# Kernel tuning notes

Measured on AMD Instinct MI355X. Metric: run time of the kernel, lower is better.

## Reference

```python
import jax, jax.numpy as jnp
import numpy as np

N_P, E_P = 50000, 400000
N_L, E_L = 50000, 400000
B = 256  # number of graphs per side
NEG_GAT = 0.2   # GATv2 leaky-relu slope
NEG_FC = 0.01   # nn.LeakyReLU default slope


def _gatv2(x, ei, Wl, Wr, att, b, H, C):
    """GATv2Conv (concat heads, add_self_loops=True). Wl/Wr: [in, H*C], att: [H, C], b: [H*C]."""
    N = x.shape[0]
    sl = jnp.arange(N)
    src = jnp.concatenate([ei[0], sl])
    dst = jnp.concatenate([ei[1], sl])
    xl = (x @ Wl).reshape(N, H, C)   # source transform (messages)
    xr = (x @ Wr).reshape(N, H, C)   # target transform
    e = jax.nn.leaky_relu(xl[src] + xr[dst], NEG_GAT)          # [E+N, H, C]
    logits = jnp.einsum('ehc,hc->eh', e, att)                   # [E+N, H]
    m = jax.ops.segment_max(logits, dst, num_segments=N)        # segment softmax
    a = jnp.exp(logits - m[dst])
    alpha = a / jax.ops.segment_sum(a, dst, num_segments=N)[dst]
    out = jax.ops.segment_sum(xl[src] * alpha[..., None], dst, num_segments=N)
    return out.reshape(N, H * C) + b


def _mean_pool(x, batch, nb):
    s = jax.ops.segment_sum(x, batch, num_segments=nb)
    c = jax.ops.segment_sum(jnp.ones((x.shape[0],), x.dtype), batch, num_segments=nb)
    return s / jnp.maximum(c, 1.0)[:, None]


def setup_inputs() -> dict:
    key = jax.random.key(0)
    ks = jax.random.split(key, 48)
    i = [0]
    def nrm(shape, fan_in):
        k = ks[i[0]]; i[0] += 1
        return jax.random.normal(k, shape, jnp.float32) / np.sqrt(fan_in)
    inp = {}
    inp['protein_x'] = jax.random.normal(ks[40], (N_P, 10), jnp.float32)
    inp['ligand_x'] = jax.random.normal(ks[41], (N_L, 5), jnp.float32)
    inp['protein_edge_index'] = jax.random.randint(ks[42], (2, E_P), 0, N_P)
    inp['ligand_edge_index'] = jax.random.randint(ks[43], (2, E_L), 0, N_L)
    inp['protein_batch'] = (jnp.arange(N_P) * B) // N_P  # sorted graph ids, all segments nonempty
    inp['ligand_batch'] = (jnp.arange(N_L) * B) // N_L
    # GATv2 params: layer1 heads=2 out=128, layer2 heads=1 out=256
    inp['p1_Wl'] = nrm((10, 256), 10); inp['p1_Wr'] = nrm((10, 256), 10)
    inp['p1_att'] = nrm((2, 128), 128); inp['p1_b'] = jnp.zeros((256,), jnp.float32)
    inp['p2_Wl'] = nrm((256, 256), 256); inp['p2_Wr'] = nrm((256, 256), 256)
    inp['p2_att'] = nrm((1, 256), 256); inp['p2_b'] = jnp.zeros((256,), jnp.float32)
    inp['l1_Wl'] = nrm((5, 256), 5); inp['l1_Wr'] = nrm((5, 256), 5)
    inp['l1_att'] = nrm((2, 128), 128); inp['l1_b'] = jnp.zeros((256,), jnp.float32)
    inp['l2_Wl'] = nrm((256, 256), 256); inp['l2_Wr'] = nrm((256, 256), 256)
    inp['l2_att'] = nrm((1, 256), 256); inp['l2_b'] = jnp.zeros((256,), jnp.float32)
    # MultiheadAttention(256, 4) params ([in, out] convention)
    inp['Wq'] = nrm((256, 256), 256); inp['bq'] = jnp.zeros((256,), jnp.float32)
    inp['Wk'] = nrm((256, 256), 256); inp['bk'] = jnp.zeros((256,), jnp.float32)
    inp['Wv'] = nrm((256, 256), 256); inp['bv'] = jnp.zeros((256,), jnp.float32)
    inp['Wo'] = nrm((256, 256), 256); inp['bo'] = jnp.zeros((256,), jnp.float32)
    # fc head
    inp['fc1_w'] = nrm((512, 256), 512); inp['fc1_b'] = jnp.zeros((256,), jnp.float32)
    inp['ln_g'] = jnp.ones((256,), jnp.float32); inp['ln_b'] = jnp.zeros((256,), jnp.float32)
    inp['fc2_w'] = nrm((256, 1), 256); inp['fc2_b'] = jnp.zeros((1,), jnp.float32)
    return inp


def reference(protein_x, protein_edge_index, protein_batch,
              ligand_x, ligand_edge_index, ligand_batch,
              p1_Wl, p1_Wr, p1_att, p1_b, p2_Wl, p2_Wr, p2_att, p2_b,
              l1_Wl, l1_Wr, l1_att, l1_b, l2_Wl, l2_Wr, l2_att, l2_b,
              Wq, bq, Wk, bk, Wv, bv, Wo, bo,
              fc1_w, fc1_b, ln_g, ln_b, fc2_w, fc2_b):
    px = _gatv2(protein_x, protein_edge_index, p1_Wl, p1_Wr, p1_att, p1_b, 2, 128)
    px = _gatv2(px, protein_edge_index, p2_Wl, p2_Wr, p2_att, p2_b, 1, 256)
    px = _mean_pool(px, protein_batch, B)                        # [B, 256]
    lx = _gatv2(ligand_x, ligand_edge_index, l1_Wl, l1_Wr, l1_att, l1_b, 2, 128)
    lx = _gatv2(lx, ligand_edge_index, l2_Wl, l2_Wr, l2_att, l2_b, 1, 256)
    lx = _mean_pool(lx, ligand_batch, B)                         # [B, 256]
    # cross attention with q/k/v seq length 1
    D, H = 256, 4
    d = D // H
    qh = (px @ Wq + bq).reshape(B, H, d)
    kh = (lx @ Wk + bk).reshape(B, H, d)
    vh = (lx @ Wv + bv).reshape(B, H, d)
    scores = (qh * kh).sum(-1) / jnp.sqrt(jnp.float32(d))        # [B, H], 1 key
    w = jax.nn.softmax(scores[..., None], axis=-1)               # all ones (single key)
    attn = (w * vh).reshape(B, D) @ Wo + bo                      # [B, 256]
    comb = jnp.concatenate([px, attn], axis=1)                   # [B, 512]
    h = comb @ fc1_w + fc1_b
    mu = h.mean(-1, keepdims=True)
    var = h.var(-1, keepdims=True)
    h = (h - mu) / jnp.sqrt(var + 1e-5) * ln_g + ln_b
    h = jax.nn.leaky_relu(h, NEG_FC)
    return h @ fc2_w + fc2_b                                     # [B, 1]
```

## Files before the change

kernel.cpp:

```cpp
#include <hip/hip_runtime.h>
#include <math.h>

typedef unsigned short u16;
typedef __attribute__((ext_vector_type(8))) short bf16x8;
typedef __attribute__((ext_vector_type(4))) float f32x4;

__device__ inline u16 f2bf(float x) {
  unsigned int u = __float_as_uint(x);
  u += 0x7fffu + ((u >> 16) & 1u);
  return (u16)(u >> 16);
}
__device__ inline float bf2f(u16 h) {
  return __uint_as_float(((unsigned int)h) << 16);
}
__device__ inline float4 ld_bf4(const u16* p) {
  ushort4 v = *(const ushort4*)p;
  return make_float4(bf2f(v.x), bf2f(v.y), bf2f(v.z), bf2f(v.w));
}

__global__ void k_setup(int* __restrict__ cnt, int nz,
                        const float* __restrict__ Wpl, const float* __restrict__ Wpr,
                        const float* __restrict__ Wll, const float* __restrict__ Wlr,
                        u16* __restrict__ Whp, u16* __restrict__ Wlp,
                        u16* __restrict__ Whl, u16* __restrict__ Wll_o) {
  const int zb = (nz + 255) / 256;
  if ((int)blockIdx.x < zb) {
    int i = blockIdx.x * 256 + threadIdx.x;
    if (i < nz) cnt[i] = 0;
    return;
  }
  int wb = blockIdx.x - zb;
  int n = wb & 511;
  int side = wb >> 9;
  int col = n & 255;
  int k = threadIdx.x;
  const float* W = side == 0 ? (n < 256 ? Wpl : Wpr) : (n < 256 ? Wll : Wlr);
  float w = W[k * 256 + col];
  u16* Wh = side ? Whl : Whp;
  u16* Wlo = side ? Wll_o : Wlp;
  u16 hb = f2bf(w);
  Wh[n * 256 + k] = hb;
  Wlo[n * 256 + k] = f2bf(w - bf2f(hb));
}

__global__ void k_histb(const int* __restrict__ eip, int Ep, const int* __restrict__ eil,
                        int El, int* __restrict__ cntp, int* __restrict__ cntl) {
  int e = blockIdx.x * blockDim.x + threadIdx.x;
  if (e < Ep) atomicAdd(&cntp[eip[Ep + e]], 1);
  else if (e < Ep + El) { int e2 = e - Ep; atomicAdd(&cntl[eil[El + e2]], 1); }
}

__global__ void k_scan1b(const int* __restrict__ cntp, int Np, const int* __restrict__ cntl,
                         int Nl, int nbp, int* __restrict__ offsp, int* __restrict__ offsl,
                         int* __restrict__ curp, int* __restrict__ curl,
                         int* __restrict__ bsum) {
  __shared__ int s[256];
  int tid = threadIdx.x;
  int side = ((int)blockIdx.x >= nbp) ? 1 : 0;
  int blk = side ? (blockIdx.x - nbp) : blockIdx.x;
  const int* cnt = side ? cntl : cntp;
  int* offs = side ? offsl : offsp;
  int* cur = side ? curl : curp;
  int N = side ? Nl : Np;
  int i = blk * 256 + tid;
  int v = (i < N) ? cnt[i] : 0;
  if (i < N) cur[i] = 0;
  s[tid] = v;
  __syncthreads();
  for (int off = 1; off < 256; off <<= 1) {
    int t = 0;
    if (tid >= off) t = s[tid - off];
    __syncthreads();
    if (tid >= off) s[tid] += t;
    __syncthreads();
  }
  if (i < N) offs[i] = s[tid] - v;
  if (tid == 255) bsum[side * 256 + blk] = s[255];
}

__global__ void k_scan2b(int* __restrict__ bsum, int nbp, int nbl) {
  __shared__ int s[256];
  int side = blockIdx.x;
  int nb = side ? nbl : nbp;
  int* bs = bsum + side * 256;
  int tid = threadIdx.x;
  int v = (tid < nb) ? bs[tid] : 0;
  s[tid] = v;
  __syncthreads();
  for (int off = 1; off < 256; off <<= 1) {
    int t = 0;
    if (tid >= off) t = s[tid - off];
    __syncthreads();
    if (tid >= off) s[tid] += t;
    __syncthreads();
  }
  if (tid < nb) bs[tid] = s[tid] - v;
}

__global__ void k_fillb(const int* __restrict__ eip, int Ep, const int* __restrict__ eil,
                        int El, const int* __restrict__ offsp, const int* __restrict__ offsl,
                        const int* __restrict__ bsum,
                        int* __restrict__ curp, int* __restrict__ curl,
                        int* __restrict__ csrp, int* __restrict__ csrl) {
  int e = blockIdx.x * blockDim.x + threadIdx.x;
  if (e < Ep) {
    int d = eip[Ep + e];
    int pos = offsp[d] + bsum[d >> 8] + atomicAdd(&curp[d], 1);
    csrp[pos] = eip[e];
  } else if (e < Ep + El) {
    int e2 = e - Ep;
    int d = eil[El + e2];
    int pos = offsl[d] + bsum[256 + (d >> 8)] + atomicAdd(&curl[d], 1);
    csrl[pos] = eil[e2];
  }
}

__global__ void k_lin_small_b(const float* __restrict__ xp, int Kp, int Np,
                              const float* __restrict__ xl_, int Kl, int Nl,
                              const float* __restrict__ Wpl, const float* __restrict__ Wpr,
                              const float* __restrict__ Wll, const float* __restrict__ Wlr,
                              u16* __restrict__ xlh_p, u16* __restrict__ xrh_p,
                              u16* __restrict__ xlh_l, u16* __restrict__ xrh_l) {
  const int side = blockIdx.y;
  const float* x = side ? xl_ : xp;
  const int K = side ? Kl : Kp;
  const int N = side ? Nl : Np;
  const float* Wl = side ? Wll : Wpl;
  const float* Wr = side ? Wlr : Wpr;
  u16* xlh = side ? xlh_l : xlh_p;
  u16* xrh = side ? xrh_l : xrh_p;
  int base = blockIdx.x * 8;
  if (base >= N) return;
  int j = threadIdx.x;
  __shared__ float xs[8][16];
  int tot = 8 * K;
  for (int i = j; i < tot; i += 256) {
    int r = i / K, k = i - r * K;
    if (base + r < N) xs[r][k] = x[(size_t)(base + r) * K + k];
  }
  __syncthreads();
#pragma unroll
  for (int r = 0; r < 8; ++r) {
    int n = base + r;
    if (n >= N) break;
    float al = 0.f, ar = 0.f;
    for (int k = 0; k < K; ++k) {
      float xv = xs[r][k];
      al = fmaf(xv, Wl[k * 256 + j], al);
      ar = fmaf(xv, Wr[k * 256 + j], ar);
    }
    xlh[(size_t)n * 256 + j] = f2bf(al);
    xrh[(size_t)n * 256 + j] = f2bf(ar);
  }
}

__global__ void __launch_bounds__(256, 2) k_mm_dual_b(
    const u16* __restrict__ A_p, const u16* __restrict__ A_l,
    const u16* __restrict__ Bh_p, const u16* __restrict__ Bl_p,
    const u16* __restrict__ Bh_l, const u16* __restrict__ Bl_l,
    u16* __restrict__ XLh_p, u16* __restrict__ XRh_p,
    u16* __restrict__ XLh_l, u16* __restrict__ XRh_l, int Np, int Nl) {
  __shared__ __align__(16) char smem[32768];
  char* sA = smem;
  char* sBh = smem + 8192;
  char* sBl = smem + 16384;
  const int side = blockIdx.z;
  const u16* A = side ? A_l : A_p;
  const u16* Bhi = side ? Bh_l : Bh_p;
  const u16* Blo = side ? Bl_l : Bl_p;
  u16* XLh = side ? XLh_l : XLh_p;
  u16* XRh = side ? XRh_l : XRh_p;
  const int M = side ? Nl : Np;
  const int t = threadIdx.x;
  const int rowBase = blockIdx.x * 128;
  if (rowBase >= M) return;
  const int j0 = blockIdx.y * 128;
  const int srow = t >> 1;
  const int h = t & 1;
  int gr = rowBase + srow;
  if (gr >= M) gr = M - 1;
  const size_t gaBase = (size_t)gr * 256 + h * 16;
  const size_t gbBase = (size_t)(j0 + srow) * 256 + h * 16;
  const int rb = srow * 64;
  const int sw0 = (((h * 2) + (srow >> 1)) & 3) * 16;
  const int sw1 = (((h * 2 + 1) + (srow >> 1)) & 3) * 16;
  const int lane = t & 63;
  const int wid = t >> 6;
  const int wm = (wid & 1) * 64;
  const int wn = (wid >> 1) * 64;
  const int kq = lane >> 4;
  const int mr = lane & 15;
  int offA[4], offB[4];
#pragma unroll
  for (int i = 0; i < 4; ++i) {
    int m = wm + i * 16 + mr;
    offA[i] = m * 64 + ((kq + (m >> 1)) & 3) * 16;
    int n = wn + i * 16 + mr;
    offB[i] = n * 64 + ((kq + (n >> 1)) & 3) * 16;
  }
  f32x4 acc[4][4] = {};
  for (int kt = 0; kt < 8; ++kt) {
    const int k0 = kt * 32;
    uint4 va0 = *(const uint4*)(A + gaBase + k0);
    uint4 va1 = *(const uint4*)(A + gaBase + k0 + 8);
    uint4 vbh0 = *(const uint4*)(Bhi + gbBase + k0);
    uint4 vbh1 = *(const uint4*)(Bhi + gbBase + k0 + 8);
    uint4 vbl0 = *(const uint4*)(Blo + gbBase + k0);
    uint4 vbl1 = *(const uint4*)(Blo + gbBase + k0 + 8);
    __syncthreads();
    *(uint4*)(sA + rb + sw0) = va0;
    *(uint4*)(sA + rb + sw1) = va1;
    *(uint4*)(sBh + rb + sw0) = vbh0;
    *(uint4*)(sBh + rb + sw1) = vbh1;
    *(uint4*)(sBl + rb + sw0) = vbl0;
    *(uint4*)(sBl + rb + sw1) = vbl1;
    __syncthreads();
    bf16x8 a[4], bh[4], bl[4];
#pragma unroll
    for (int i = 0; i < 4; ++i) {
      a[i] = *(const bf16x8*)(sA + offA[i]);
      bh[i] = *(const bf16x8*)(sBh + offB[i]);
      bl[i] = *(const bf16x8*)(sBl + offB[i]);
    }
#pragma unroll
    for (int i = 0; i < 4; ++i)
#pragma unroll
      for (int j = 0; j < 4; ++j) {
        acc[i][j] = __builtin_amdgcn_mfma_f32_16x16x32_bf16(a[i], bh[j], acc[i][j], 0, 0, 0);
        acc[i][j] = __builtin_amdgcn_mfma_f32_16x16x32_bf16(a[i], bl[j], acc[i][j], 0, 0, 0);
      }
  }
  __syncthreads();
  u16* wtile = (u16*)(smem + wid * 8192);
#pragma unroll
  for (int i = 0; i < 4; ++i)
#pragma unroll
    for (int j = 0; j < 4; ++j)
#pragma unroll
      for (int r = 0; r < 4; ++r)
        wtile[(i * 16 + kq * 4 + r) * 64 + j * 16 + mr] = f2bf(acc[i][j][r]);
  u16* cbase = (blockIdx.y < 2) ? XLh : XRh;
  const int cb = (blockIdx.y < 2) ? j0 : j0 - 256;
  const int r8 = lane >> 3;
  const int c8 = lane & 7;
#pragma unroll
  for (int rr = 0; rr < 8; ++rr) {
    int lr = rr * 8 + r8;
    uint4 v = *(const uint4*)&wtile[lr * 64 + c8 * 8];
    int row = rowBase + wm + lr;
    if (row < M) *(uint4*)&cbase[(size_t)row * 256 + cb + wn + c8 * 8] = v;
  }
}

#define GAT_DOT(a, q)                                                        \
  {                                                                          \
    float t0 = a.x + rd.x, t1 = a.y + rd.y, t2 = a.z + rd.z, t3 = a.w + rd.w; \
    q = fmaf(fmaxf(t0, 0.2f * t0), wa.x,                                     \
        fmaf(fmaxf(t1, 0.2f * t1), wa.y,                                     \
        fmaf(fmaxf(t2, 0.2f * t2), wa.z, fmaxf(t3, 0.2f * t3) * wa.w)));     \
  }

template <int H>
__global__ void k_gat_gather_b(
    const u16* __restrict__ xlh_p, const u16* __restrict__ xrh_p, u16* __restrict__ out_p,
    const u16* __restrict__ xlh_l, const u16* __restrict__ xrh_l, u16* __restrict__ out_l,
    const int* __restrict__ csr_p, const int* __restrict__ offs_p,
    const int* __restrict__ cnt_p,
    const int* __restrict__ csr_l, const int* __restrict__ offs_l,
    const int* __restrict__ cnt_l, const int* __restrict__ bsum,
    const float* __restrict__ att_p, const float* __restrict__ bias_p,
    const float* __restrict__ att_l, const float* __restrict__ bias_l,
    int Np, int Nl) {
  const int side = blockIdx.y;
  const u16* xlh = side ? xlh_l : xlh_p;
  const u16* xrh = side ? xrh_l : xrh_p;
  u16* out = side ? out_l : out_p;
  const int* csr = side ? csr_l : csr_p;
  const int* offs = side ? offs_l : offs_p;
  const int* cnt = side ? cnt_l : cnt_p;
  const float* att = side ? att_l : att_p;
  const float* bias = side ? bias_l : bias_p;
  const int N = side ? Nl : Np;
  int d = blockIdx.x * 4 + (threadIdx.x >> 6);
  if (d >= N) return;
  const int lo4 = (threadIdx.x & 63) * 4;
  const float4 rd = ld_bf4(&xrh[(size_t)d * 256 + lo4]);
  const float4 wa = *(const float4*)&att[lo4];
  const float4 xd = ld_bf4(&xlh[(size_t)d * 256 + lo4]);
  float base;
  GAT_DOT(xd, base)
#pragma unroll
  for (int off = 1; off <= (H == 2 ? 16 : 32); off <<= 1) base += __shfl_xor(base, off, 64);
  float l0 = 1.f, l1 = 0.f, l2 = 0.f, l3 = 0.f;
  float4 acc0 = xd;
  float4 acc1 = make_float4(0.f, 0.f, 0.f, 0.f);
  float4 acc2 = make_float4(0.f, 0.f, 0.f, 0.f);
  float4 acc3 = make_float4(0.f, 0.f, 0.f, 0.f);
  const int o0 = offs[d] + bsum[side * 256 + (d >> 8)];
  const int c = cnt[d];
  int j = 0;
  for (; j + 3 < c; j += 4) {
    int s0 = csr[o0 + j], s1 = csr[o0 + j + 1], s2 = csr[o0 + j + 2], s3 = csr[o0 + j + 3];
    float4 a0 = ld_bf4(&xlh[(size_t)s0 * 256 + lo4]);
    float4 a1 = ld_bf4(&xlh[(size_t)s1 * 256 + lo4]);
    float4 a2 = ld_bf4(&xlh[(size_t)s2 * 256 + lo4]);
    float4 a3 = ld_bf4(&xlh[(size_t)s3 * 256 + lo4]);
    float q0, q1, q2, q3;
    GAT_DOT(a0, q0)
    GAT_DOT(a1, q1)
    GAT_DOT(a2, q2)
    GAT_DOT(a3, q3)
#pragma unroll
    for (int off = 1; off <= (H == 2 ? 16 : 32); off <<= 1) {
      q0 += __shfl_xor(q0, off, 64);
      q1 += __shfl_xor(q1, off, 64);
      q2 += __shfl_xor(q2, off, 64);
      q3 += __shfl_xor(q3, off, 64);
    }
    float w0 = __expf(q0 - base), w1 = __expf(q1 - base);
    float w2 = __expf(q2 - base), w3 = __expf(q3 - base);
    l0 += w0; l1 += w1; l2 += w2; l3 += w3;
    acc0.x = fmaf(w0, a0.x, acc0.x); acc0.y = fmaf(w0, a0.y, acc0.y);
    acc0.z = fmaf(w0, a0.z, acc0.z); acc0.w = fmaf(w0, a0.w, acc0.w);
    acc1.x = fmaf(w1, a1.x, acc1.x); acc1.y = fmaf(w1, a1.y, acc1.y);
    acc1.z = fmaf(w1, a1.z, acc1.z); acc1.w = fmaf(w1, a1.w, acc1.w);
    acc2.x = fmaf(w2, a2.x, acc2.x); acc2.y = fmaf(w2, a2.y, acc2.y);
    acc2.z = fmaf(w2, a2.z, acc2.z); acc2.w = fmaf(w2, a2.w, acc2.w);
    acc3.x = fmaf(w3, a3.x, acc3.x); acc3.y = fmaf(w3, a3.y, acc3.y);
    acc3.z = fmaf(w3, a3.z, acc3.z); acc3.w = fmaf(w3, a3.w, acc3.w);
  }
  for (; j < c; ++j) {
    int s0 = csr[o0 + j];
    float4 a0 = ld_bf4(&xlh[(size_t)s0 * 256 + lo4]);
    float q0;
    GAT_DOT(a0, q0)
#pragma unroll
    for (int off = 1; off <= (H == 2 ? 16 : 32); off <<= 1) q0 += __shfl_xor(q0, off, 64);
    float w0 = __expf(q0 - base);
    l0 += w0;
    acc0.x = fmaf(w0, a0.x, acc0.x); acc0.y = fmaf(w0, a0.y, acc0.y);
    acc0.z = fmaf(w0, a0.z, acc0.z); acc0.w = fmaf(w0, a0.w, acc0.w);
  }
  float inv = 1.f / (l0 + l1 + l2 + l3);
  float ax = acc0.x + acc1.x + acc2.x + acc3.x;
  float ay = acc0.y + acc1.y + acc2.y + acc3.y;
  float az = acc0.z + acc1.z + acc2.z + acc3.z;
  float aw = acc0.w + acc1.w + acc2.w + acc3.w;
  const float4 b4 = *(const float4*)&bias[lo4];
  ushort4 hv;
  hv.x = f2bf(ax * inv + b4.x);
  hv.y = f2bf(ay * inv + b4.y);
  hv.z = f2bf(az * inv + b4.z);
  hv.w = f2bf(aw * inv + b4.w);
  *(ushort4*)&out[(size_t)d * 256 + lo4] = hv;
}

#define POOL_C 8
__global__ void k_pool_part(const u16* __restrict__ xp, const int* __restrict__ bp, int Np,
                            const u16* __restrict__ xl_, const int* __restrict__ bl_, int Nl,
                            float* __restrict__ PPpart, float* __restrict__ LPpart) {
  const int b = blockIdx.x;
  const int side = blockIdx.y;
  const int chunk = blockIdx.z;
  const u16* x = side ? xl_ : xp;
  const int* batch = side ? bl_ : bp;
  const int N = side ? Nl : Np;
  float* part = side ? LPpart : PPpart;
  int j = threadIdx.x;
  __shared__ int sss, sse;
  if (j == 0) {
    int lo = 0, hi = N;
    while (lo < hi) { int mid = (lo + hi) >> 1; if (batch[mid] < b) lo = mid + 1; else hi = mid; }
    sss = lo;
    lo = 0; hi = N;
    while (lo < hi) { int mid = (lo + hi) >> 1; if (batch[mid] < b + 1) lo = mid + 1; else hi = mid; }
    sse = lo;
  }
  __syncthreads();
  int len = sse - sss;
  int per = (len + POOL_C - 1) / POOL_C;
  int st = sss + chunk * per;
  int en = st + per;
  if (en > sse) en = sse;
  float acc = 0.f;
  for (int n = st; n < en; ++n) acc += bf2f(x[(size_t)n * 256 + j]);
  part[((size_t)chunk * 256 + b) * 256 + j] = acc;
}

__global__ void k_head(const float* __restrict__ PPpart, const float* __restrict__ LPpart,
                       const int* __restrict__ bp, int Np,
                       const int* __restrict__ bl_, int Nl,
                       const float* __restrict__ Wv, const float* __restrict__ bv,
                       const float* __restrict__ Wo, const float* __restrict__ bo,
                       const float* __restrict__ fc1w, const float* __restrict__ fc1b,
                       const float* __restrict__ lng, const float* __restrict__ lnb,
                       const float* __restrict__ fc2w, const float* __restrict__ fc2b,
                       float* __restrict__ out) {
  int b = blockIdx.x;
  int j = threadIdx.x;
  __shared__ float lxs[256];
  __shared__ float vbuf[256];
  __shared__ float comb[512];
  __shared__ float r1[256], r2[256];
  __shared__ float smu, srs;
  __shared__ int seg[4];
  if (j < 2) {
    const int* batch = j ? bl_ : bp;
    int N = j ? Nl : Np;
    int lo = 0, hi = N;
    while (lo < hi) { int mid = (lo + hi) >> 1; if (batch[mid] < b) lo = mid + 1; else hi = mid; }
    seg[j * 2] = lo;
    lo = 0; hi = N;
    while (lo < hi) { int mid = (lo + hi) >> 1; if (batch[mid] < b + 1) lo = mid + 1; else hi = mid; }
    seg[j * 2 + 1] = lo;
  }
  __syncthreads();
  {
    float accp = 0.f, accl = 0.f;
#pragma unroll
    for (int c = 0; c < POOL_C; ++c) {
      accp += PPpart[((size_t)c * 256 + b) * 256 + j];
      accl += LPpart[((size_t)c * 256 + b) * 256 + j];
    }
    comb[j] = accp / fmaxf((float)(seg[1] - seg[0]), 1.f);
    lxs[j] = accl / fmaxf((float)(seg[3] - seg[2]), 1.f);
  }
  __syncthreads();
  float v = bv[j];
  for (int k = 0; k < 256; ++k) v = fmaf(lxs[k], Wv[k * 256 + j], v);
  vbuf[j] = v;
  __syncthreads();
  float at = bo[j];
  for (int k = 0; k < 256; ++k) at = fmaf(vbuf[k], Wo[k * 256 + j], at);
  comb[256 + j] = at;
  __syncthreads();
  float h = fc1b[j];
  for (int k = 0; k < 512; ++k) h = fmaf(comb[k], fc1w[k * 256 + j], h);
  r1[j] = h;
  r2[j] = h * h;
  __syncthreads();
  for (int off = 128; off > 0; off >>= 1) {
    if (j < off) { r1[j] += r1[j + off]; r2[j] += r2[j + off]; }
    __syncthreads();
  }
  if (j == 0) {
    float mu = r1[0] / 256.f;
    float var = r2[0] / 256.f - mu * mu;
    smu = mu;
    srs = 1.f / sqrtf(var + 1e-5f);
  }
  __syncthreads();
  float hn = (h - smu) * srs * lng[j] + lnb[j];
  hn = hn > 0.f ? hn : 0.01f * hn;
  r1[j] = hn * fc2w[j];
  __syncthreads();
  for (int off = 128; off > 0; off >>= 1) {
    if (j < off) r1[j] += r1[j + off];
    __syncthreads();
  }
  if (j == 0) out[b] = r1[0] + fc2b[0];
}

extern "C" void kernel_launch(void* const* d_in, const int* in_sizes, int n_in,
                              void* d_out, int out_size, void* d_ws, size_t ws_size,
                              hipStream_t stream) {
  const float* px = (const float*)d_in[0];
  const float* lx = (const float*)d_in[1];
  const int* pei = (const int*)d_in[2];
  const int* lei = (const int*)d_in[3];
  const int* pb = (const int*)d_in[4];
  const int* lb = (const int*)d_in[5];
  const float* p1_Wl = (const float*)d_in[6];
  const float* p1_Wr = (const float*)d_in[7];
  const float* p1_att = (const float*)d_in[8];
  const float* p1_b = (const float*)d_in[9];
  const float* p2_Wl = (const float*)d_in[10];
  const float* p2_Wr = (const float*)d_in[11];
  const float* p2_att = (const float*)d_in[12];
  const float* p2_b = (const float*)d_in[13];
  const float* l1_Wl = (const float*)d_in[14];
  const float* l1_Wr = (const float*)d_in[15];
  const float* l1_att = (const float*)d_in[16];
  const float* l1_b = (const float*)d_in[17];
  const float* l2_Wl = (const float*)d_in[18];
  const float* l2_Wr = (const float*)d_in[19];
  const float* l2_att = (const float*)d_in[20];
  const float* l2_b = (const float*)d_in[21];
  const float* Wv = (const float*)d_in[26];
  const float* bv = (const float*)d_in[27];
  const float* Wo = (const float*)d_in[28];
  const float* bo = (const float*)d_in[29];
  const float* fc1w = (const float*)d_in[30];
  const float* fc1b = (const float*)d_in[31];
  const float* lng = (const float*)d_in[32];
  const float* lnb = (const float*)d_in[33];
  const float* fc2w = (const float*)d_in[34];
  const float* fc2b = (const float*)d_in[35];

  const int NPn = in_sizes[4];
  const int NLn = in_sizes[5];
  const int EPe = in_sizes[2] / 2;
  const int ELe = in_sizes[3] / 2;
  const int KP = in_sizes[0] / NPn;
  const int KL = in_sizes[1] / NLn;

  const int Nmax = NPn > NLn ? NPn : NLn;
  const int Emax = EPe > ELe ? EPe : ELe;
  size_t NF = (size_t)Nmax * 256;

  u16* XLh_p = (u16*)d_ws;
  u16* XRh_p = XLh_p + NF;
  u16* Ah_p = XRh_p + NF;
  u16* XLh_l = Ah_p + NF;
  u16* XRh_l = XLh_l + NF;
  u16* Ah_l = XRh_l + NF;
  u16* Wth = Ah_l + NF;
  u16* Wtl = Wth + 2 * 512 * 256;
  float* PPpart = (float*)(Wtl + 2 * 512 * 256);
  float* LPpart = PPpart + (size_t)POOL_C * 256 * 256;
  int* cnt = (int*)(LPpart + (size_t)POOL_C * 256 * 256);
  int* cur = cnt + 2 * (size_t)Nmax;
  int* offs = cur + 2 * (size_t)Nmax;
  int* bsum = offs + 2 * (size_t)Nmax;
  int* csr = bsum + 512;
  int* cnt_l = cnt + Nmax;
  int* cur_l = cur + Nmax;
  int* offs_l = offs + Nmax;
  int* csr_l = csr + Emax;

  const int nbp = (NPn + 255) / 256;
  const int nbl = (NLn + 255) / 256;
  const int nz = 2 * Nmax;
  const int zb = (nz + 255) / 256;

  k_setup<<<zb + 1024, 256, 0, stream>>>(cnt, nz, p2_Wl, p2_Wr, l2_Wl, l2_Wr,
                                         Wth, Wtl, Wth + 512 * 256, Wtl + 512 * 256);
  k_histb<<<(EPe + ELe + 255) / 256, 256, 0, stream>>>(pei, EPe, lei, ELe, cnt, cnt_l);
  k_scan1b<<<nbp + nbl, 256, 0, stream>>>(cnt, NPn, cnt_l, NLn, nbp, offs, offs_l,
                                          cur, cur_l, bsum);
  k_scan2b<<<2, 256, 0, stream>>>(bsum, nbp, nbl);
  k_fillb<<<(EPe + ELe + 255) / 256, 256, 0, stream>>>(pei, EPe, lei, ELe, offs, offs_l,
                                                       bsum, cur, cur_l, csr, csr_l);
  k_lin_small_b<<<dim3((Nmax + 7) / 8, 2), 256, 0, stream>>>(
      px, KP, NPn, lx, KL, NLn, p1_Wl, p1_Wr, l1_Wl, l1_Wr,
      XLh_p, XRh_p, XLh_l, XRh_l);
  k_gat_gather_b<2><<<dim3((Nmax + 3) / 4, 2), 256, 0, stream>>>(
      XLh_p, XRh_p, Ah_p, XLh_l, XRh_l, Ah_l,
      csr, offs, cnt, csr_l, offs_l, cnt_l, bsum,
      p1_att, p1_b, l1_att, l1_b, NPn, NLn);
  k_mm_dual_b<<<dim3((Nmax + 127) / 128, 4, 2), 256, 0, stream>>>(
      Ah_p, Ah_l, Wth, Wtl, Wth + 512 * 256, Wtl + 512 * 256,
      XLh_p, XRh_p, XLh_l, XRh_l, NPn, NLn);
  k_gat_gather_b<1><<<dim3((Nmax + 3) / 4, 2), 256, 0, stream>>>(
      XLh_p, XRh_p, Ah_p, XLh_l, XRh_l, Ah_l,
      csr, offs, cnt, csr_l, offs_l, cnt_l, bsum,
      p2_att, p2_b, l2_att, l2_b, NPn, NLn);
  k_pool_part<<<dim3(256, 2, POOL_C), 256, 0, stream>>>(Ah_p, pb, NPn, Ah_l, lb, NLn,
                                                        PPpart, LPpart);
  k_head<<<256, 256, 0, stream>>>(PPpart, LPpart, pb, NPn, lb, NLn,
                                  Wv, bv, Wo, bo, fc1w, fc1b, lng, lnb, fc2w, fc2b,
                                  (float*)d_out);
  (void)n_in; (void)out_size; (void)ws_size;
}
```

Before: 596.8 us.

## Widen GEMM N-tile to 256 and rewrite GATv2 leaky-relu dot via abs identity

The dual-bf16 GEMM block now computes a 128x256 output tile instead of 128x128, halving the grid's N dimension. This lets each A tile be reused across twice as many columns, and each warp now holds a 4x8 accumulator array with a two-chunk epilogue. The cost is more registers and more shared memory per block, which may cut occupancy. Separately, the leaky-relu-times-attention dot is rewritten as 0.6*t + 0.4*|t|, with scaled attention weights precomputed, so it uses fewer ALU ops in the gather loop.

```diff
diff --git a/kernel.cpp b/kernel.cpp
--- a/kernel.cpp
+++ b/kernel.cpp
@@ -160,104 +160,116 @@
     const u16* __restrict__ Bh_l, const u16* __restrict__ Bl_l,
     u16* __restrict__ XLh_p, u16* __restrict__ XRh_p,
     u16* __restrict__ XLh_l, u16* __restrict__ XRh_l, int Np, int Nl) {
-  __shared__ __align__(16) char smem[32768];
+  __shared__ __align__(16) char smem[40960];
   char* sA = smem;
   char* sBh = smem + 8192;
-  char* sBl = smem + 16384;
+  char* sBl = smem + 24576;
   const int side = blockIdx.z;
   const u16* A = side ? A_l : A_p;
   const u16* Bhi = side ? Bh_l : Bh_p;
   const u16* Blo = side ? Bl_l : Bl_p;
-  u16* XLh = side ? XLh_l : XLh_p;
-  u16* XRh = side ? XRh_l : XRh_p;
   const int M = side ? Nl : Np;
   const int t = threadIdx.x;
   const int rowBase = blockIdx.x * 128;
   if (rowBase >= M) return;
-  const int j0 = blockIdx.y * 128;
+  const int nsel = blockIdx.y;
   const int srow = t >> 1;
   const int h = t & 1;
   int gr = rowBase + srow;
   if (gr >= M) gr = M - 1;
   const size_t gaBase = (size_t)gr * 256 + h * 16;
-  const size_t gbBase = (size_t)(j0 + srow) * 256 + h * 16;
-  const int rb = srow * 64;
-  const int sw0 = (((h * 2) + (srow >> 1)) & 3) * 16;
-  const int sw1 = (((h * 2 + 1) + (srow >> 1)) & 3) * 16;
+  const int rbA = srow * 64;
+  const int swA0 = (((h * 2) + (srow >> 1)) & 3) * 16;
+  const int swA1 = (((h * 2 + 1) + (srow >> 1)) & 3) * 16;
+  const size_t gbBase = (size_t)(nsel * 256 + t) * 256;
+  const int rbB = t * 64;
+  int swB[4];
+#pragma unroll
+  for (int q = 0; q < 4; ++q) swB[q] = ((q + (t >> 1)) & 3) * 16;
   const int lane = t & 63;
   const int wid = t >> 6;
   const int wm = (wid & 1) * 64;
-  const int wn = (wid >> 1) * 64;
+  const int wn = (wid >> 1) * 128;
   const int kq = lane >> 4;
   const int mr = lane & 15;
-  int offA[4], offB[4];
+  int offA[4], offB[8];
 #pragma unroll
   for (int i = 0; i < 4; ++i) {
     int m = wm + i * 16 + mr;
     offA[i] = m * 64 + ((kq + (m >> 1)) & 3) * 16;
-    int n = wn + i * 16 + mr;
-    offB[i] = n * 64 + ((kq + (n >> 1)) & 3) * 16;
-  }
-  f32x4 acc[4][4] = {};
+  }
+#pragma unroll
+  for (int j = 0; j < 8; ++j) {
+    int n = wn + j * 16 + mr;
+    offB[j] = n * 64 + ((kq + (n >> 1)) & 3) * 16;
+  }
+  f32x4 acc[4][8] = {};
   for (int kt = 0; kt < 8; ++kt) {
     const int k0 = kt * 32;
     uint4 va0 = *(const uint4*)(A + gaBase + k0);
     uint4 va1 = *(const uint4*)(A + gaBase + k0 + 8);
-    uint4 vbh0 = *(const uint4*)(Bhi + gbBase + k0);
-    uint4 vbh1 = *(const uint4*)(Bhi + gbBase + k0 + 8);
-    uint4 vbl0 = *(const uint4*)(Blo + gbBase + k0);
-    uint4 vbl1 = *(const uint4*)(Blo + gbBase + k0 + 8);
-    __syncthreads();
-    *(uint4*)(sA + rb + sw0) = va0;
-    *(uint4*)(sA + rb + sw1) = va1;
-    *(uint4*)(sBh + rb + sw0) = vbh0;
-    *(uint4*)(sBh + rb + sw1) = vbh1;
-    *(uint4*)(sBl + rb + sw0) = vbl0;
-    *(uint4*)(sBl + rb + sw1) = vbl1;
-    __syncthreads();
-    bf16x8 a[4], bh[4], bl[4];
-#pragma unroll
-    for (int i = 0; i < 4; ++i) {
-      a[i] = *(const bf16x8*)(sA + offA[i]);
-      bh[i] = *(const bf16x8*)(sBh + offB[i]);
-      bl[i] = *(const bf16x8*)(sBl + offB[i]);
-    }
-#pragma unroll
-    for (int i = 0; i < 4; ++i)
-#pragma unroll
-      for (int j = 0; j < 4; ++j) {
-        acc[i][j] = __builtin_amdgcn_mfma_f32_16x16x32_bf16(a[i], bh[j], acc[i][j], 0, 0, 0);
-        acc[i][j] = __builtin_amdgcn_mfma_f32_16x16x32_bf16(a[i], bl[j], acc[i][j], 0, 0, 0);
+    uint4 vbh[4], vbl[4];
+#pragma unroll
+    for (int q = 0; q < 4; ++q) {
+      vbh[q] = *(const uint4*)(Bhi + gbBase + k0 + q * 8);
+      vbl[q] = *(const uint4*)(Blo + gbBase + k0 + q * 8);
+    }
+    __syncthreads();
+    *(uint4*)(sA + rbA + swA0) = va0;
+    *(uint4*)(sA + rbA + swA1) = va1;
+#pragma unroll
+    for (int q = 0; q < 4; ++q) {
+      *(uint4*)(sBh + rbB + swB[q]) = vbh[q];
+      *(uint4*)(sBl + rbB + swB[q]) = vbl[q];
+    }
+    __syncthreads();
+    bf16x8 a[4];
+#pragma unroll
+    for (int i = 0; i < 4; ++i) a[i] = *(const bf16x8*)(sA + offA[i]);
+#pragma unroll
+    for (int j = 0; j < 8; ++j) {
+      bf16x8 bh = *(const bf16x8*)(sBh + offB[j]);
+      bf16x8 bl = *(const bf16x8*)(sBl + offB[j]);
+#pragma unroll
+      for (int i = 0; i < 4; ++i) {
+        acc[i][j] = __builtin_amdgcn_mfma_f32_16x16x32_bf16(a[i], bh, acc[i][j], 0, 0, 0);
+        acc[i][j] = __builtin_amdgcn_mfma_f32_16x16x32_bf16(a[i], bl, acc[i][j], 0, 0, 0);
       }
+    }
   }
   __syncthreads();
   u16* wtile = (u16*)(smem + wid * 8192);
-#pragma unroll
-  for (int i = 0; i < 4; ++i)
-#pragma unroll
-    for (int j = 0; j < 4; ++j)
-#pragma unroll
-      for (int r = 0; r < 4; ++r)
-        wtile[(i * 16 + kq * 4 + r) * 64 + j * 16 + mr] = f2bf(acc[i][j][r]);
-  u16* cbase = (blockIdx.y < 2) ? XLh : XRh;
-  const int cb = (blockIdx.y < 2) ? j0 : j0 - 256;
+  u16* cbase = nsel ? (side ? XRh_l : XRh_p) : (side ? XLh_l : XLh_p);
   const int r8 = lane >> 3;
   const int c8 = lane & 7;
 #pragma unroll
-  for (int rr = 0; rr < 8; ++rr) {
-    int lr = rr * 8 + r8;
-    uint4 v = *(const uint4*)&wtile[lr * 64 + c8 * 8];
-    int row = rowBase + wm + lr;
-    if (row < M) *(uint4*)&cbase[(size_t)row * 256 + cb + wn + c8 * 8] = v;
-  }
-}
-
-#define GAT_DOT(a, q)                                                        \
-  {                                                                          \
-    float t0 = a.x + rd.x, t1 = a.y + rd.y, t2 = a.z + rd.z, t3 = a.w + rd.w; \
-    q = fmaf(fmaxf(t0, 0.2f * t0), wa.x,                                     \
-        fmaf(fmaxf(t1, 0.2f * t1), wa.y,                                     \
-        fmaf(fmaxf(t2, 0.2f * t2), wa.z, fmaxf(t3, 0.2f * t3) * wa.w)));     \
+  for (int ch = 0; ch < 2; ++ch) {
+#pragma unroll
+    for (int i = 0; i < 4; ++i)
+#pragma unroll
+      for (int jj = 0; jj < 4; ++jj) {
+        int j = ch * 4 + jj;
+#pragma unroll
+        for (int r = 0; r < 4; ++r)
+          wtile[(i * 16 + kq * 4 + r) * 64 + jj * 16 + mr] = f2bf(acc[i][j][r]);
+      }
+#pragma unroll
+    for (int rr = 0; rr < 8; ++rr) {
+      int lr = rr * 8 + r8;
+      uint4 v = *(const uint4*)&wtile[lr * 64 + c8 * 8];
+      int row = rowBase + wm + lr;
+      if (row < M) *(uint4*)&cbase[(size_t)row * 256 + wn + ch * 64 + c8 * 8] = v;
+    }
+  }
+}
+
+#define GAT_DOT(a, q)                                                          \
+  {                                                                            \
+    float t0 = a.x + rd.x, t1 = a.y + rd.y, t2 = a.z + rd.z, t3 = a.w + rd.w;  \
+    q = fmaf(t3, wa6.w, fabsf(t3) * wa4.w);                                    \
+    q = fmaf(fabsf(t2), wa4.z, fmaf(t2, wa6.z, q));                            \
+    q = fmaf(fabsf(t1), wa4.y, fmaf(t1, wa6.y, q));                            \
+    q = fmaf(fabsf(t0), wa4.x, fmaf(t0, wa6.x, q));                            \
   }
 
 template <int H>
@@ -286,6 +298,8 @@
   const int lo4 = (threadIdx.x & 63) * 4;
   const float4 rd = ld_bf4(&xrh[(size_t)d * 256 + lo4]);
   const float4 wa = *(const float4*)&att[lo4];
+  const float4 wa6 = make_float4(0.6f * wa.x, 0.6f * wa.y, 0.6f * wa.z, 0.6f * wa.w);
+  const float4 wa4 = make_float4(0.4f * wa.x, 0.4f * wa.y, 0.4f * wa.z, 0.4f * wa.w);
   const float4 xd = ld_bf4(&xlh[(size_t)d * 256 + lo4]);
   float base;
   GAT_DOT(xd, base)
@@ -548,7 +562,7 @@
       XLh_p, XRh_p, Ah_p, XLh_l, XRh_l, Ah_l,
       csr, offs, cnt, csr_l, offs_l, cnt_l, bsum,
       p1_att, p1_b, l1_att, l1_b, NPn, NLn);
-  k_mm_dual_b<<<dim3((Nmax + 127) / 128, 4, 2), 256, 0, stream>>>(
+  k_mm_dual_b<<<dim3((Nmax + 127) / 128, 2, 2), 256, 0, stream>>>(
       Ah_p, Ah_l, Wth, Wtl, Wth + 512 * 256, Wtl + 512 * 256,
       XLh_p, XRh_p, XLh_l, XRh_l, NPn, NLn);
   k_gat_gather_b<1><<<dim3((Nmax + 3) / 4, 2), 256, 0, stream>>>(
```

Result: slower. 688.5 us (+15.4%).
